# Kernel optimization log

Hardware: AMD Instinct MI355X
Metric: run time of the kernel (lower is better)

Reference implementation:

```python
import jax, jax.numpy as jnp
import numpy as np

MARGIN = 0.2  # from init_kwargs
N, D, N_CLASSES = 8192, 256, 64


def setup_inputs() -> dict:
    key = jax.random.key(0)
    k1, k2 = jax.random.split(key)
    embeddings = jax.random.normal(k1, (N, D), dtype=jnp.float32)
    targets = jax.random.randint(k2, (N,), 0, N_CLASSES, dtype=jnp.int64)
    return {"embeddings": embeddings, "targets": targets}


def _mine_triplets(embeddings, targets):
    sq = jnp.sum(embeddings * embeddings, axis=1)  # [N]
    dist = -2.0 * (embeddings @ embeddings.T) + sq[None, :] + sq[:, None]  # [N, N]
    pos_mask = targets[:, None] == targets[None, :]  # same label (incl. self, as in original)
    NEG_INF = jnp.asarray(-1e30, dist.dtype)
    POS_INF = jnp.asarray(1e30, dist.dtype)
    hardest_pos = jnp.argmax(jnp.where(pos_mask, dist, NEG_INF), axis=1)  # [N]
    hardest_neg = jnp.argmin(jnp.where(pos_mask, POS_INF, dist), axis=1)  # [N]
    anchors = jnp.arange(targets.shape[0])
    return jnp.stack([anchors, hardest_pos, hardest_neg], axis=1)  # [N, 3]


def reference(embeddings, targets):
    triplets = _mine_triplets(embeddings, targets)
    a, p, n = triplets[:, 0], triplets[:, 1], triplets[:, 2]
    ap = jnp.sum((embeddings[a] - embeddings[p]) ** 2, axis=1)
    an = jnp.sum((embeddings[a] - embeddings[n]) ** 2, axis=1)
    losses = jax.nn.relu(ap - an + MARGIN)
    return losses.mean(), triplets
```

## Files before the change

kernel.cpp:

```cpp
#include <hip/hip_runtime.h>

#define NROWS 8192
#define DDIM 256
#define MARGIN_F 0.2f
#define CSPLIT 32

typedef _Float16 half8 __attribute__((ext_vector_type(8)));
typedef float f32x4 __attribute__((ext_vector_type(4)));
typedef int i32x4 __attribute__((ext_vector_type(4)));

__device__ __forceinline__ void gld16(const void* g, void* l) {
  __builtin_amdgcn_global_load_lds(
      (const __attribute__((address_space(1))) void*)g,
      (__attribute__((address_space(3))) void*)l, 16, 0, 0);
}

__global__ __launch_bounds__(256)
void prep_kernel(const float* __restrict__ E, _Float16* __restrict__ Eh,
                 _Float16* __restrict__ El, float* __restrict__ sq) {
  const int t = threadIdx.x;
  const int r = t >> 4;
  const int cs = t & 15;
  const int rg = blockIdx.x;
  const int row = rg * 16 + r;
  const float* src = &E[row * DDIM + cs * 16];
  float s = 0.f;
  half8 H[2], L[2];
#pragma unroll
  for (int h = 0; h < 2; ++h) {
    const float4 f0 = *(const float4*)(src + h * 8);
    const float4 f1 = *(const float4*)(src + h * 8 + 4);
    const float v[8] = {f0.x, f0.y, f0.z, f0.w, f1.x, f1.y, f1.z, f1.w};
#pragma unroll
    for (int e = 0; e < 8; ++e) {
      s = fmaf(v[e], v[e], s);
      const _Float16 hi = (_Float16)v[e];
      H[h][e] = hi;
      L[h][e] = (_Float16)(v[e] - (float)hi);
    }
  }
  const int kt = cs >> 1;
  const int g0 = (cs & 1) * 2;
  const int base = (rg * 8 + kt) * 512;
  *(half8*)&Eh[base + g0 * 128 + r * 8] = H[0];
  *(half8*)&Eh[base + (g0 + 1) * 128 + r * 8] = H[1];
  *(half8*)&El[base + g0 * 128 + r * 8] = L[0];
  *(half8*)&El[base + (g0 + 1) * 128 + r * 8] = L[1];
#pragma unroll
  for (int o = 8; o > 0; o >>= 1) s += __shfl_down(s, o, 16);
  if (cs == 0) sq[row] = s;
}

__global__ __launch_bounds__(512, 2)
void mine_kernel(const _Float16* __restrict__ Eh, const _Float16* __restrict__ El,
                 const int* __restrict__ T, const float* __restrict__ sq,
                 float* __restrict__ pv, int* __restrict__ pi,
                 float* __restrict__ nv, int* __restrict__ ni) {
  __shared__ __align__(16) _Float16 S[2][4][8192];

  const int tid = threadIdx.x;
  const int lane = tid & 63;
  const int w = tid >> 6;
  const int wi = w >> 1, wj = w & 1;
  const int l15 = lane & 15, grp = lane >> 4;
  const int rowbase = blockIdx.y * 256;
  const int colbase = blockIdx.x * 256;

  const int arr = w >> 1;
  const int shalf = w & 1;
  const _Float16* sA = (arr & 1) ? El : Eh;
  const int rgb = (((arr < 2) ? rowbase : colbase) >> 4) + shalf * 8;

  float sqi[4]; int ti[4];
#pragma unroll
  for (int fi = 0; fi < 4; ++fi) {
    const int i = rowbase + wi * 64 + fi * 16 + l15;
    sqi[fi] = sq[i];
    ti[fi] = T[i];
  }

  float bpv[4], bnv[4]; int bpi[4], bni[4];
#pragma unroll
  for (int fi = 0; fi < 4; ++fi) { bpv[fi] = -3e38f; bnv[fi] = 3e38f; bpi[fi] = 0; bni[fi] = 0; }

  f32x4 acc[8][4];
#pragma unroll
  for (int jf = 0; jf < 8; ++jf)
#pragma unroll
    for (int fi = 0; fi < 4; ++fi) acc[jf][fi] = (f32x4){0.f, 0.f, 0.f, 0.f};

#pragma unroll
  for (int t = 0; t < 8; ++t)
    gld16(sA + ((rgb + t) * 8 + 0) * 512 + lane * 8, &S[0][arr][(shalf * 8 + t) * 512]);
  __syncthreads();

  for (int kt = 0; kt < 8; ++kt) {
    const int cur = kt & 1;
    if (kt < 7) {
#pragma unroll
      for (int t = 0; t < 8; ++t)
        gld16(sA + ((rgb + t) * 8 + kt + 1) * 512 + lane * 8,
              &S[cur ^ 1][arr][(shalf * 8 + t) * 512]);
    }
#pragma unroll
    for (int jh = 0; jh < 2; ++jh) {
      half8 ajh[4], ajl[4];
#pragma unroll
      for (int jf = 0; jf < 4; ++jf) {
        const int rg = wj * 8 + jh * 4 + jf;
        ajh[jf] = *(const half8*)&S[cur][2][rg * 512 + lane * 8];
        ajl[jf] = *(const half8*)&S[cur][3][rg * 512 + lane * 8];
      }
#pragma unroll
      for (int fi = 0; fi < 4; ++fi) {
        const half8 bh = *(const half8*)&S[cur][0][(wi * 4 + fi) * 512 + lane * 8];
        const half8 bl = *(const half8*)&S[cur][1][(wi * 4 + fi) * 512 + lane * 8];
        __builtin_amdgcn_s_setprio(1);
#pragma unroll
        for (int jf = 0; jf < 4; ++jf)
          acc[jh * 4 + jf][fi] = __builtin_amdgcn_mfma_f32_16x16x32_f16(ajh[jf], bh, acc[jh * 4 + jf][fi], 0, 0, 0);
#pragma unroll
        for (int jf = 0; jf < 4; ++jf)
          acc[jh * 4 + jf][fi] = __builtin_amdgcn_mfma_f32_16x16x32_f16(ajl[jf], bh, acc[jh * 4 + jf][fi], 0, 0, 0);
#pragma unroll
        for (int jf = 0; jf < 4; ++jf)
          acc[jh * 4 + jf][fi] = __builtin_amdgcn_mfma_f32_16x16x32_f16(ajh[jf], bl, acc[jh * 4 + jf][fi], 0, 0, 0);
        __builtin_amdgcn_s_setprio(0);
      }
    }
    __syncthreads();
  }

#pragma unroll
  for (int jf = 0; jf < 8; ++jf) {
    const int jb = colbase + wj * 128 + jf * 16 + grp * 4;
    const f32x4 sqj = *(const f32x4*)&sq[jb];
    const i32x4 tj = *(const i32x4*)&T[jb];
#pragma unroll
    for (int fi = 0; fi < 4; ++fi) {
#pragma unroll
      for (int r = 0; r < 4; ++r) {
        const float dst = fmaf(-2.f, acc[jf][fi][r], sqi[fi] + sqj[r]);
        const int jidx = jb + r;
        if (ti[fi] == tj[r]) {
          if (dst > bpv[fi]) { bpv[fi] = dst; bpi[fi] = jidx; }
        } else {
          if (dst < bnv[fi]) { bnv[fi] = dst; bni[fi] = jidx; }
        }
      }
    }
  }

#pragma unroll
  for (int fi = 0; fi < 4; ++fi) {
#pragma unroll
    for (int off = 16; off <= 32; off <<= 1) {
      const float ov = __shfl_xor(bpv[fi], off, 64);
      const int oi = __shfl_xor(bpi[fi], off, 64);
      if (ov > bpv[fi] || (ov == bpv[fi] && oi < bpi[fi])) { bpv[fi] = ov; bpi[fi] = oi; }
      const float on = __shfl_xor(bnv[fi], off, 64);
      const int oni = __shfl_xor(bni[fi], off, 64);
      if (on < bnv[fi] || (on == bnv[fi] && oni < bni[fi])) { bnv[fi] = on; bni[fi] = oni; }
    }
  }

  float4* scr = (float4*)&S[0][0][0];
  if (wj == 1 && lane < 16) {
#pragma unroll
    for (int fi = 0; fi < 4; ++fi)
      scr[wi * 64 + fi * 16 + lane] =
          make_float4(bpv[fi], __int_as_float(bpi[fi]), bnv[fi], __int_as_float(bni[fi]));
  }
  __syncthreads();
  if (wj == 0 && lane < 16) {
#pragma unroll
    for (int fi = 0; fi < 4; ++fi) {
      const float4 o = scr[wi * 64 + fi * 16 + lane];
      const int oi = __float_as_int(o.y), oni = __float_as_int(o.w);
      if (o.x > bpv[fi] || (o.x == bpv[fi] && oi < bpi[fi])) { bpv[fi] = o.x; bpi[fi] = oi; }
      if (o.z < bnv[fi] || (o.z == bnv[fi] && oni < bni[fi])) { bnv[fi] = o.z; bni[fi] = oni; }
      const int row = rowbase + wi * 64 + fi * 16 + lane;
      const int oidx = row * CSPLIT + blockIdx.x;
      pv[oidx] = bpv[fi]; pi[oidx] = bpi[fi]; nv[oidx] = bnv[fi]; ni[oidx] = bni[fi];
    }
  }
}

__global__ __launch_bounds__(256)
void finish_kernel(const float* __restrict__ E,
                   const float* __restrict__ pv, const int* __restrict__ pi,
                   const float* __restrict__ nv, const int* __restrict__ ni,
                   float* __restrict__ out, float* __restrict__ bl) {
  const int w = threadIdx.x >> 6, lane = threadIdx.x & 63;
  const int row = blockIdx.x * 4 + w;
  float Pv = -3e38f, Nv = 3e38f; int Pi = 0, Ni = 0;
#pragma unroll
  for (int s = 0; s < CSPLIT; ++s) {
    const float p = pv[row * CSPLIT + s]; const int px = pi[row * CSPLIT + s];
    if (p > Pv || (p == Pv && px < Pi)) { Pv = p; Pi = px; }
    const float n = nv[row * CSPLIT + s]; const int nx = ni[row * CSPLIT + s];
    if (n < Nv || (n == Nv && nx < Ni)) { Nv = n; Ni = nx; }
  }
  const float4 a = *(const float4*)&E[row * DDIM + lane * 4];
  const float4 p4 = *(const float4*)&E[Pi * DDIM + lane * 4];
  const float4 n4 = *(const float4*)&E[Ni * DDIM + lane * 4];
  float ap = (a.x - p4.x) * (a.x - p4.x) + (a.y - p4.y) * (a.y - p4.y)
           + (a.z - p4.z) * (a.z - p4.z) + (a.w - p4.w) * (a.w - p4.w);
  float an = (a.x - n4.x) * (a.x - n4.x) + (a.y - n4.y) * (a.y - n4.y)
           + (a.z - n4.z) * (a.z - n4.z) + (a.w - n4.w) * (a.w - n4.w);
#pragma unroll
  for (int o = 32; o > 0; o >>= 1) {
    ap += __shfl_down(ap, o, 64);
    an += __shfl_down(an, o, 64);
  }
  __shared__ float ls[4];
  if (lane == 0) {
    out[1 + row * 3 + 0] = (float)row;
    out[1 + row * 3 + 1] = (float)Pi;
    out[1 + row * 3 + 2] = (float)Ni;
    ls[w] = fmaxf(ap - an + MARGIN_F, 0.f);
  }
  __syncthreads();
  if (threadIdx.x == 0) bl[blockIdx.x] = (ls[0] + ls[1]) + (ls[2] + ls[3]);
}

__global__ __launch_bounds__(256)
void sum_kernel(const float* __restrict__ bl, float* __restrict__ out) {
  __shared__ float s[256];
  float t = 0.f;
#pragma unroll
  for (int r = 0; r < (NROWS / 4) / 256; ++r) t += bl[threadIdx.x + r * 256];
  s[threadIdx.x] = t;
  __syncthreads();
  for (int o = 128; o > 0; o >>= 1) {
    if (threadIdx.x < o) s[threadIdx.x] += s[threadIdx.x + o];
    __syncthreads();
  }
  if (threadIdx.x == 0) out[0] = s[0] * (1.f / NROWS);
}

extern "C" void kernel_launch(void* const* d_in, const int* in_sizes, int n_in,
                              void* d_out, int out_size, void* d_ws, size_t ws_size,
                              hipStream_t stream) {
  const float* E = (const float*)d_in[0];
  const int* T = (const int*)d_in[1];
  float* out = (float*)d_out;

  _Float16* Eh = (_Float16*)d_ws;
  _Float16* El = Eh + NROWS * DDIM;
  float* sq = (float*)(El + NROWS * DDIM);
  float* pv = sq + NROWS;
  int*   pi = (int*)(pv + NROWS * CSPLIT);
  float* nv = (float*)(pi + NROWS * CSPLIT);
  int*   ni = (int*)(nv + NROWS * CSPLIT);
  float* bl = (float*)(ni + NROWS * CSPLIT);

  prep_kernel<<<NROWS / 16, 256, 0, stream>>>(E, Eh, El, sq);
  mine_kernel<<<dim3(NROWS / 256, NROWS / 256), 512, 0, stream>>>(Eh, El, T, sq, pv, pi, nv, ni);
  finish_kernel<<<NROWS / 4, 256, 0, stream>>>(E, pv, pi, nv, ni, out, bl);
  sum_kernel<<<1, 256, 0, stream>>>(bl, out);
}
```

Baseline: 151.7 us.

## Switch mining GEMM to 32x32x16 MFMA with matching fragment layout

Replaces the 16x16x32 f16 MFMA tiles with 32x32x16 tiles, which reduces the number of MFMA instructions and LDS fragment loads per output and gives larger per-wave accumulator fragments. The prep kernel is rewritten to emit the 32-row fragment layout, and sums row norms through shared memory instead of shuffles. The K loop is split into two half-steps with their own prefetch, wrapped in extra s_barriers, and the epilogue reduction is adapted to the new accumulator layout. The extra barriers add synchronisation cost, and the changed interleaving could reduce load/compute overlap.

```diff
diff --git a/kernel.cpp b/kernel.cpp
--- a/kernel.cpp
+++ b/kernel.cpp
@@ -7,6 +7,7 @@
 
 typedef _Float16 half8 __attribute__((ext_vector_type(8)));
 typedef float f32x4 __attribute__((ext_vector_type(4)));
+typedef float f32x16 __attribute__((ext_vector_type(16)));
 typedef int i32x4 __attribute__((ext_vector_type(4)));
 
 __device__ __forceinline__ void gld16(const void* g, void* l) {
@@ -18,37 +19,42 @@
 __global__ __launch_bounds__(256)
 void prep_kernel(const float* __restrict__ E, _Float16* __restrict__ Eh,
                  _Float16* __restrict__ El, float* __restrict__ sq) {
+  __shared__ float scratch[256];
   const int t = threadIdx.x;
-  const int r = t >> 4;
-  const int cs = t & 15;
+  const int r = t & 31;
+  const int kseg = t >> 5;
   const int rg = blockIdx.x;
-  const int row = rg * 16 + r;
-  const float* src = &E[row * DDIM + cs * 16];
+  const int row = rg * 32 + r;
+  const float* src = &E[row * DDIM + kseg * 32];
   float s = 0.f;
-  half8 H[2], L[2];
-#pragma unroll
-  for (int h = 0; h < 2; ++h) {
-    const float4 f0 = *(const float4*)(src + h * 8);
-    const float4 f1 = *(const float4*)(src + h * 8 + 4);
+#pragma unroll
+  for (int sub = 0; sub < 4; ++sub) {
+    const float4 f0 = *(const float4*)(src + sub * 8);
+    const float4 f1 = *(const float4*)(src + sub * 8 + 4);
     const float v[8] = {f0.x, f0.y, f0.z, f0.w, f1.x, f1.y, f1.z, f1.w};
+    half8 H, L;
 #pragma unroll
     for (int e = 0; e < 8; ++e) {
       s = fmaf(v[e], v[e], s);
       const _Float16 hi = (_Float16)v[e];
-      H[h][e] = hi;
-      L[h][e] = (_Float16)(v[e] - (float)hi);
-    }
-  }
-  const int kt = cs >> 1;
-  const int g0 = (cs & 1) * 2;
-  const int base = (rg * 8 + kt) * 512;
-  *(half8*)&Eh[base + g0 * 128 + r * 8] = H[0];
-  *(half8*)&Eh[base + (g0 + 1) * 128 + r * 8] = H[1];
-  *(half8*)&El[base + g0 * 128 + r * 8] = L[0];
-  *(half8*)&El[base + (g0 + 1) * 128 + r * 8] = L[1];
-#pragma unroll
-  for (int o = 8; o > 0; o >>= 1) s += __shfl_down(s, o, 16);
-  if (cs == 0) sq[row] = s;
+      H[e] = hi;
+      L[e] = (_Float16)(v[e] - (float)hi);
+    }
+    const int k0 = kseg * 32 + sub * 8;
+    const int kt = k0 >> 4;
+    const int g = (k0 >> 3) & 1;
+    const int dst = (rg * 16 + kt) * 512 + g * 256 + r * 8;
+    *(half8*)&Eh[dst] = H;
+    *(half8*)&El[dst] = L;
+  }
+  scratch[t] = s;
+  __syncthreads();
+  if (t < 32) {
+    float acc = 0.f;
+#pragma unroll
+    for (int seg = 0; seg < 8; ++seg) acc += scratch[seg * 32 + t];
+    sq[rg * 32 + t] = acc;
+  }
 }
 
 __global__ __launch_bounds__(512, 2)
@@ -62,124 +68,133 @@
   const int lane = tid & 63;
   const int w = tid >> 6;
   const int wi = w >> 1, wj = w & 1;
-  const int l15 = lane & 15, grp = lane >> 4;
+  const int l31 = lane & 31;
   const int rowbase = blockIdx.y * 256;
   const int colbase = blockIdx.x * 256;
 
   const int arr = w >> 1;
   const int shalf = w & 1;
   const _Float16* sA = (arr & 1) ? El : Eh;
-  const int rgb = (((arr < 2) ? rowbase : colbase) >> 4) + shalf * 8;
-
-  float sqi[4]; int ti[4];
-#pragma unroll
-  for (int fi = 0; fi < 4; ++fi) {
-    const int i = rowbase + wi * 64 + fi * 16 + l15;
+  const int rgb = ((arr < 2) ? blockIdx.y : blockIdx.x) * 8;
+
+  float sqi[2]; int ti[2];
+#pragma unroll
+  for (int fi = 0; fi < 2; ++fi) {
+    const int i = rowbase + wi * 64 + fi * 32 + l31;
     sqi[fi] = sq[i];
     ti[fi] = T[i];
   }
 
-  float bpv[4], bnv[4]; int bpi[4], bni[4];
-#pragma unroll
-  for (int fi = 0; fi < 4; ++fi) { bpv[fi] = -3e38f; bnv[fi] = 3e38f; bpi[fi] = 0; bni[fi] = 0; }
-
-  f32x4 acc[8][4];
-#pragma unroll
-  for (int jf = 0; jf < 8; ++jf)
-#pragma unroll
-    for (int fi = 0; fi < 4; ++fi) acc[jf][fi] = (f32x4){0.f, 0.f, 0.f, 0.f};
-
-#pragma unroll
-  for (int t = 0; t < 8; ++t)
-    gld16(sA + ((rgb + t) * 8 + 0) * 512 + lane * 8, &S[0][arr][(shalf * 8 + t) * 512]);
-  __syncthreads();
-
-  for (int kt = 0; kt < 8; ++kt) {
-    const int cur = kt & 1;
-    if (kt < 7) {
-#pragma unroll
-      for (int t = 0; t < 8; ++t)
-        gld16(sA + ((rgb + t) * 8 + kt + 1) * 512 + lane * 8,
-              &S[cur ^ 1][arr][(shalf * 8 + t) * 512]);
-    }
-#pragma unroll
-    for (int jh = 0; jh < 2; ++jh) {
+  float bpv[2], bnv[2]; int bpi[2], bni[2];
+#pragma unroll
+  for (int fi = 0; fi < 2; ++fi) { bpv[fi] = -3e38f; bnv[fi] = 3e38f; bpi[fi] = 0; bni[fi] = 0; }
+
+  f32x16 acc[4][2];
+#pragma unroll
+  for (int jf = 0; jf < 4; ++jf)
+#pragma unroll
+    for (int fi = 0; fi < 2; ++fi) acc[jf][fi] = (f32x16)(0.f);
+
+#pragma unroll
+  for (int c = 0; c < 8; ++c)
+    gld16(sA + ((rgb + shalf * 4 + (c >> 1)) * 16 + (c & 1)) * 512 + lane * 8,
+          &S[0][arr][((shalf * 4 + (c >> 1)) * 2 + (c & 1)) * 512]);
+  __syncthreads();
+
+  for (int ktg = 0; ktg < 8; ++ktg) {
+    const int cur = ktg & 1;
+#pragma unroll
+    for (int p = 0; p < 2; ++p) {
+      if (ktg < 7) {
+#pragma unroll
+        for (int cc = 0; cc < 4; ++cc) {
+          const int c = p * 4 + cc;
+          gld16(sA + ((rgb + shalf * 4 + (c >> 1)) * 16 + (ktg + 1) * 2 + (c & 1)) * 512 + lane * 8,
+                &S[cur ^ 1][arr][((shalf * 4 + (c >> 1)) * 2 + (c & 1)) * 512]);
+        }
+      }
       half8 ajh[4], ajl[4];
 #pragma unroll
       for (int jf = 0; jf < 4; ++jf) {
-        const int rg = wj * 8 + jh * 4 + jf;
-        ajh[jf] = *(const half8*)&S[cur][2][rg * 512 + lane * 8];
-        ajl[jf] = *(const half8*)&S[cur][3][rg * 512 + lane * 8];
-      }
-#pragma unroll
-      for (int fi = 0; fi < 4; ++fi) {
-        const half8 bh = *(const half8*)&S[cur][0][(wi * 4 + fi) * 512 + lane * 8];
-        const half8 bl = *(const half8*)&S[cur][1][(wi * 4 + fi) * 512 + lane * 8];
-        __builtin_amdgcn_s_setprio(1);
-#pragma unroll
-        for (int jf = 0; jf < 4; ++jf)
-          acc[jh * 4 + jf][fi] = __builtin_amdgcn_mfma_f32_16x16x32_f16(ajh[jf], bh, acc[jh * 4 + jf][fi], 0, 0, 0);
-#pragma unroll
-        for (int jf = 0; jf < 4; ++jf)
-          acc[jh * 4 + jf][fi] = __builtin_amdgcn_mfma_f32_16x16x32_f16(ajl[jf], bh, acc[jh * 4 + jf][fi], 0, 0, 0);
-#pragma unroll
-        for (int jf = 0; jf < 4; ++jf)
-          acc[jh * 4 + jf][fi] = __builtin_amdgcn_mfma_f32_16x16x32_f16(ajh[jf], bl, acc[jh * 4 + jf][fi], 0, 0, 0);
-        __builtin_amdgcn_s_setprio(0);
-      }
+        const int o = ((wj * 4 + jf) * 2 + p) * 512 + lane * 8;
+        ajh[jf] = *(const half8*)&S[cur][2][o];
+        ajl[jf] = *(const half8*)&S[cur][3][o];
+      }
+      half8 bh[2], bl[2];
+#pragma unroll
+      for (int fi = 0; fi < 2; ++fi) {
+        const int o = ((wi * 2 + fi) * 2 + p) * 512 + lane * 8;
+        bh[fi] = *(const half8*)&S[cur][0][o];
+        bl[fi] = *(const half8*)&S[cur][1][o];
+      }
+      __builtin_amdgcn_s_barrier();
+      __builtin_amdgcn_s_setprio(1);
+#pragma unroll
+      for (int fi = 0; fi < 2; ++fi)
+#pragma unroll
+        for (int jf = 0; jf < 4; ++jf) {
+          acc[jf][fi] = __builtin_amdgcn_mfma_f32_32x32x16_f16(ajh[jf], bh[fi], acc[jf][fi], 0, 0, 0);
+          acc[jf][fi] = __builtin_amdgcn_mfma_f32_32x32x16_f16(ajl[jf], bh[fi], acc[jf][fi], 0, 0, 0);
+          acc[jf][fi] = __builtin_amdgcn_mfma_f32_32x32x16_f16(ajh[jf], bl[fi], acc[jf][fi], 0, 0, 0);
+        }
+      __builtin_amdgcn_s_setprio(0);
+      __builtin_amdgcn_s_barrier();
     }
     __syncthreads();
   }
 
-#pragma unroll
-  for (int jf = 0; jf < 8; ++jf) {
-    const int jb = colbase + wj * 128 + jf * 16 + grp * 4;
-    const f32x4 sqj = *(const f32x4*)&sq[jb];
-    const i32x4 tj = *(const i32x4*)&T[jb];
-#pragma unroll
-    for (int fi = 0; fi < 4; ++fi) {
-#pragma unroll
-      for (int r = 0; r < 4; ++r) {
-        const float dst = fmaf(-2.f, acc[jf][fi][r], sqi[fi] + sqj[r]);
-        const int jidx = jb + r;
-        if (ti[fi] == tj[r]) {
-          if (dst > bpv[fi]) { bpv[fi] = dst; bpi[fi] = jidx; }
-        } else {
-          if (dst < bnv[fi]) { bnv[fi] = dst; bni[fi] = jidx; }
+  const int lh4 = (lane >> 5) * 4;
+#pragma unroll
+  for (int jf = 0; jf < 4; ++jf) {
+    const int jfbase = colbase + wj * 128 + jf * 32;
+#pragma unroll
+    for (int q = 0; q < 4; ++q) {
+      const int jb = jfbase + 8 * q + lh4;
+      const f32x4 sqj = *(const f32x4*)&sq[jb];
+      const i32x4 tj = *(const i32x4*)&T[jb];
+#pragma unroll
+      for (int fi = 0; fi < 2; ++fi) {
+#pragma unroll
+        for (int rr = 0; rr < 4; ++rr) {
+          const float dst = fmaf(-2.f, acc[jf][fi][q * 4 + rr], sqi[fi] + sqj[rr]);
+          const int jidx = jb + rr;
+          if (ti[fi] == tj[rr]) {
+            if (dst > bpv[fi]) { bpv[fi] = dst; bpi[fi] = jidx; }
+          } else {
+            if (dst < bnv[fi]) { bnv[fi] = dst; bni[fi] = jidx; }
+          }
         }
       }
     }
   }
 
 #pragma unroll
-  for (int fi = 0; fi < 4; ++fi) {
-#pragma unroll
-    for (int off = 16; off <= 32; off <<= 1) {
-      const float ov = __shfl_xor(bpv[fi], off, 64);
-      const int oi = __shfl_xor(bpi[fi], off, 64);
-      if (ov > bpv[fi] || (ov == bpv[fi] && oi < bpi[fi])) { bpv[fi] = ov; bpi[fi] = oi; }
-      const float on = __shfl_xor(bnv[fi], off, 64);
-      const int oni = __shfl_xor(bni[fi], off, 64);
-      if (on < bnv[fi] || (on == bnv[fi] && oni < bni[fi])) { bnv[fi] = on; bni[fi] = oni; }
-    }
-  }
-
+  for (int fi = 0; fi < 2; ++fi) {
+    const float ov = __shfl_xor(bpv[fi], 32, 64);
+    const int oi = __shfl_xor(bpi[fi], 32, 64);
+    if (ov > bpv[fi] || (ov == bpv[fi] && oi < bpi[fi])) { bpv[fi] = ov; bpi[fi] = oi; }
+    const float on = __shfl_xor(bnv[fi], 32, 64);
+    const int oni = __shfl_xor(bni[fi], 32, 64);
+    if (on < bnv[fi] || (on == bnv[fi] && oni < bni[fi])) { bnv[fi] = on; bni[fi] = oni; }
+  }
+
+  __syncthreads();
   float4* scr = (float4*)&S[0][0][0];
-  if (wj == 1 && lane < 16) {
-#pragma unroll
-    for (int fi = 0; fi < 4; ++fi)
-      scr[wi * 64 + fi * 16 + lane] =
+  if (wj == 1 && lane < 32) {
+#pragma unroll
+    for (int fi = 0; fi < 2; ++fi)
+      scr[wi * 64 + fi * 32 + l31] =
           make_float4(bpv[fi], __int_as_float(bpi[fi]), bnv[fi], __int_as_float(bni[fi]));
   }
   __syncthreads();
-  if (wj == 0 && lane < 16) {
-#pragma unroll
-    for (int fi = 0; fi < 4; ++fi) {
-      const float4 o = scr[wi * 64 + fi * 16 + lane];
+  if (wj == 0 && lane < 32) {
+#pragma unroll
+    for (int fi = 0; fi < 2; ++fi) {
+      const float4 o = scr[wi * 64 + fi * 32 + l31];
       const int oi = __float_as_int(o.y), oni = __float_as_int(o.w);
       if (o.x > bpv[fi] || (o.x == bpv[fi] && oi < bpi[fi])) { bpv[fi] = o.x; bpi[fi] = oi; }
       if (o.z < bnv[fi] || (o.z == bnv[fi] && oni < bni[fi])) { bnv[fi] = o.z; bni[fi] = oni; }
-      const int row = rowbase + wi * 64 + fi * 16 + lane;
+      const int row = rowbase + wi * 64 + fi * 32 + l31;
       const int oidx = row * CSPLIT + blockIdx.x;
       pv[oidx] = bpv[fi]; pi[oidx] = bpi[fi]; nv[oidx] = bnv[fi]; ni[oidx] = bni[fi];
     }
@@ -255,7 +270,7 @@
   int*   ni = (int*)(nv + NROWS * CSPLIT);
   float* bl = (float*)(ni + NROWS * CSPLIT);
 
-  prep_kernel<<<NROWS / 16, 256, 0, stream>>>(E, Eh, El, sq);
+  prep_kernel<<<NROWS / 32, 256, 0, stream>>>(E, Eh, El, sq);
   mine_kernel<<<dim3(NROWS / 256, NROWS / 256), 512, 0, stream>>>(Eh, El, T, sq, pv, pi, nv, ni);
   finish_kernel<<<NROWS / 4, 256, 0, stream>>>(E, pv, pi, nv, ni, out, bl);
   sum_kernel<<<1, 256, 0, stream>>>(bl, out);
```

Result: no change. 152.7 us (+0.7%).
